# Kernel tuning notes

Measured on AMD Instinct MI355X. Metric: run time of the kernel, lower is better.

Reference implementation:

```python
import jax, jax.numpy as jnp
import numpy as np

B, T, NT, H, L, F, NH, R = 2, 1024, 30, 1024, 8, 2816, 16, 16
HD = H // NH
LORA_SCALE = 32.0 / 16.0  # lora_alpha / r
CLAMP = 10.0
EPS = 1e-6


def _rms(x, w):
    return x * jax.lax.rsqrt(jnp.mean(x * x, axis=-1, keepdims=True) + EPS) * w


def _rope(x):
    # x: [B,T,NH,HD] -- LLaMA rotary embedding
    half = HD // 2
    inv_freq = 1.0 / (10000.0 ** (jnp.arange(0, half, dtype=jnp.float32) / half))
    ang = jnp.arange(x.shape[1], dtype=jnp.float32)[:, None] * inv_freq  # [T,half]
    cos = jnp.concatenate([jnp.cos(ang), jnp.cos(ang)], -1)[None, :, None, :]
    sin = jnp.concatenate([jnp.sin(ang), jnp.sin(ang)], -1)[None, :, None, :]
    x1, x2 = x[..., :half], x[..., half:]
    return x * cos + jnp.concatenate([-x2, x1], -1) * sin


def _lora(x, W, A, Bm):
    # W: [in,out], A: [r,in], Bm: [out,r]  (dequantized base + LoRA update)
    return x @ W + ((x @ A.T) @ Bm.T) * LORA_SCALE


def setup_inputs():
    key = jax.random.key(0)
    ks = jax.random.split(key, 16)
    n = lambda k, s, sc=0.02: jax.random.normal(k, s, jnp.float32) * sc
    return {
        'x': jax.random.normal(ks[0], (B, T, NT), jnp.float32),
        'temperature': jnp.float32(1.0),
        'state_W': n(ks[1], (NT, H), 0.1),
        'state_b': jnp.zeros((H,), jnp.float32),
        'ln1': jnp.ones((L, H), jnp.float32),
        'ln2': jnp.ones((L, H), jnp.float32),
        'Wqkv': n(ks[2], (L, 3, H, H)),
        'Aqkv': n(ks[3], (L, 3, R, H)),
        'Bqkv': n(ks[4], (L, 3, H, R)),
        'Wo': n(ks[5], (L, H, H)),
        'Ao': n(ks[6], (L, R, H)),
        'Bo': n(ks[7], (L, H, R)),
        'Wgu': n(ks[8], (L, 2, H, F)),
        'Agu': n(ks[9], (L, 2, R, H)),
        'Bgu': n(ks[10], (L, 2, F, R)),
        'Wd': n(ks[11], (L, F, H)),
        'Ad': n(ks[12], (L, R, F)),
        'Bd': n(ks[13], (L, H, R)),
        'ln_f': jnp.ones((H,), jnp.float32),
        'head_W': n(ks[14], (H, NT + 1), 0.01),
        'head_b': jnp.zeros((NT + 1,), jnp.float32),
    }


def reference(x, temperature, state_W, state_b, ln1, ln2, Wqkv, Aqkv, Bqkv,
              Wo, Ao, Bo, Wgu, Agu, Bgu, Wd, Ad, Bd, ln_f, head_W, head_b):
    causal = jnp.tril(jnp.ones((T, T), bool))

    def layer(h, p):
        l1, l2, wqkv, aqkv, bqkv, wo, ao, bo, wgu, agu, bgu, wd, ad, bd = p
        hn = _rms(h, l1)
        qkv = jnp.einsum('bth,khd->kbtd', hn, wqkv)
        qkv = qkv + jnp.einsum('kbtr,kdr->kbtd',
                               jnp.einsum('bth,krh->kbtr', hn, aqkv), bqkv) * LORA_SCALE
        q = _rope(qkv[0].reshape(B, T, NH, HD))
        k = _rope(qkv[1].reshape(B, T, NH, HD))
        v = qkv[2].reshape(B, T, NH, HD)
        scores = jnp.einsum('bqhd,bkhd->bhqk', q, k) / np.sqrt(HD).astype(np.float32)
        scores = jnp.where(causal, scores, jnp.float32(-1e9))
        probs = jax.nn.softmax(scores, axis=-1)
        att = jnp.einsum('bhqk,bkhd->bqhd', probs, v).reshape(B, T, H)
        h = h + _lora(att, wo, ao, bo)
        hn2 = _rms(h, l2)
        gu = jnp.einsum('bth,khf->kbtf', hn2, wgu)
        gu = gu + jnp.einsum('kbtr,kfr->kbtf',
                             jnp.einsum('bth,krh->kbtr', hn2, agu), bgu) * LORA_SCALE
        act = jax.nn.silu(gu[0]) * gu[1]
        h = h + _lora(act, wd, ad, bd)
        return h, None

    h = x @ state_W + state_b  # state encoder -> inputs_embeds
    h, _ = jax.lax.scan(layer, h, (ln1, ln2, Wqkv, Aqkv, Bqkv, Wo, Ao, Bo,
                                   Wgu, Agu, Bgu, Wd, Ad, Bd))
    latent = _rms(h, ln_f)  # last hidden state
    logits = latent @ head_W + head_b
    logits_clamped = jnp.clip(logits, -CLAMP, CLAMP)
    portfolio_weights = jax.nn.softmax(logits_clamped / temperature, axis=-1)
    return portfolio_weights, logits_clamped
```

## Files before the change

kernel.cpp:

```cpp
#include <hip/hip_runtime.h>
#include <hip/hip_bf16.h>
#include <cstdint>

#define B_    2
#define T_    1024
#define NT_   30
#define H_    1024
#define L_    8
#define F_    2816
#define NH_   16
#define R_    16
#define HD_   64
#define M_    2048
#define NTP1_ 31

typedef unsigned short u16;
typedef short  s16x8 __attribute__((ext_vector_type(8)));
typedef unsigned short u16x4 __attribute__((ext_vector_type(4)));
typedef unsigned short u16x8 __attribute__((ext_vector_type(8)));
typedef float  f32x4 __attribute__((ext_vector_type(4)));

__device__ __forceinline__ u16 f2bf(float f){
  __hip_bfloat16 h = __float2bfloat16(f);
  return __builtin_bit_cast(unsigned short, h);
}
__device__ __forceinline__ float bf2f(u16 u){
  uint32_t v = (uint32_t)u << 16;
  return __builtin_bit_cast(float, v);
}

__device__ __forceinline__ void async16(const void* g, void* l){
  __builtin_amdgcn_global_load_lds((const __attribute__((address_space(1))) void*)g,
                                   (__attribute__((address_space(3))) void*)l, 16, 0, 0);
}

__global__ __launch_bounds__(256, 3) void fold_kernel(
    const float* __restrict__ W, const float* __restrict__ A,
    const float* __restrict__ Bm, u16* __restrict__ Wt,
    int K, int N, long strW, long strA, long strB, long strWt)
{
  const int mat = blockIdx.z;
  W  += (long)mat * strW;  A  += (long)mat * strA;
  Bm += (long)mat * strB;  Wt += (long)mat * strWt;
  const int k0 = blockIdx.x * 64, n0 = blockIdx.y * 64;
  __shared__ float Wt_s[64][65];
  __shared__ float As[16][64];
  __shared__ float Bs[64][20];
  const int tid = threadIdx.x;
  {
    const int kr = tid >> 4;
    const int n4 = (tid & 15) * 4;
    #pragma unroll
    for (int p = 0; p < 4; p++){
      int krow = p * 16 + kr;
      float4 w = *(const float4*)(W + (long)(k0 + krow) * N + n0 + n4);
      Wt_s[n4+0][krow] = w.x; Wt_s[n4+1][krow] = w.y;
      Wt_s[n4+2][krow] = w.z; Wt_s[n4+3][krow] = w.w;
    }
    const int r = tid >> 4, kc = (tid & 15) * 4;
    *(float4*)&As[r][kc] = *(const float4*)(A + (long)r * K + k0 + kc);
    const int nb = tid >> 2, r4 = (tid & 3) * 4;
    float4 b = *(const float4*)(Bm + (long)(n0 + nb) * 16 + r4);
    Bs[nb][r4+0]=b.x; Bs[nb][r4+1]=b.y; Bs[nb][r4+2]=b.z; Bs[nb][r4+3]=b.w;
  }
  __syncthreads();
  const int ko = (tid & 7) * 8;
  const int na = tid >> 3;
  float bq0[16], bq1[16];
  #pragma unroll
  for (int c = 0; c < 4; c++){
    *(float4*)&bq0[c*4] = *(const float4*)&Bs[na][c*4];
    *(float4*)&bq1[c*4] = *(const float4*)&Bs[na+32][c*4];
  }
  float l0[8] = {}, l1[8] = {};
  #pragma unroll
  for (int r = 0; r < 16; r++){
    float a[8];
    *(float4*)&a[0] = *(const float4*)&As[r][ko];
    *(float4*)&a[4] = *(const float4*)&As[r][ko+4];
    #pragma unroll
    for (int j = 0; j < 8; j++){
      l0[j] += a[j] * bq0[r];
      l1[j] += a[j] * bq1[r];
    }
  }
  u16x8 o0, o1;
  #pragma unroll
  for (int j = 0; j < 8; j++){
    o0[j] = f2bf(Wt_s[na][ko+j]    + 2.0f * l0[j]);
    o1[j] = f2bf(Wt_s[na+32][ko+j] + 2.0f * l1[j]);
  }
  *(u16x8*)(Wt + (long)(n0+na)*K    + k0 + ko) = o0;
  *(u16x8*)(Wt + (long)(n0+na+32)*K + k0 + ko) = o1;
}

__global__ __launch_bounds__(256) void embed_kernel(
    const float* __restrict__ x, const float* __restrict__ sw,
    const float* __restrict__ sb, float* __restrict__ h)
{
  const int m = blockIdx.x;
  const float* xr = x + (long)m * NT_;
  for (int jj = threadIdx.x; jj < H_; jj += 256){
    float acc = sb[jj];
    #pragma unroll
    for (int i = 0; i < NT_; i++) acc += xr[i] * sw[i * H_ + jj];
    h[(long)m * H_ + jj] = acc;
  }
}

__global__ __launch_bounds__(256) void rms_kernel(
    float* __restrict__ hsrc, const u16* __restrict__ pb,
    const float* __restrict__ w, u16* __restrict__ outp, int nparts)
{
  const int m = blockIdx.x, t = threadIdx.x;
  float4 v = ((const float4*)(hsrc + (long)m * H_))[t];
  if (nparts){
    for (int k = 0; k < nparts; k++){
      u16x4 a = *(const u16x4*)(pb + (long)k * M_ * H_ + (long)m * H_ + t * 4);
      v.x += bf2f(a[0]); v.y += bf2f(a[1]); v.z += bf2f(a[2]); v.w += bf2f(a[3]);
    }
    ((float4*)(hsrc + (long)m * H_))[t] = v;
  }
  float ss = v.x*v.x + v.y*v.y + v.z*v.z + v.w*v.w;
  #pragma unroll
  for (int off = 32; off >= 1; off >>= 1) ss += __shfl_xor(ss, off);
  __shared__ float red[4];
  if ((t & 63) == 0) red[t >> 6] = ss;
  __syncthreads();
  const float scale = rsqrtf((red[0]+red[1]+red[2]+red[3]) * (1.0f/H_) + 1e-6f);
  const float4 wv = ((const float4*)w)[t];
  u16x4 o;
  o[0] = f2bf(v.x*scale*wv.x); o[1] = f2bf(v.y*scale*wv.y);
  o[2] = f2bf(v.z*scale*wv.z); o[3] = f2bf(v.w*scale*wv.w);
  *(u16x4*)(outp + (long)m * H_ + t * 4) = o;
}

template<int OUTBF>
__global__ __launch_bounds__(256, 3) void gemm_bt(
    const u16* __restrict__ Ag, const u16* __restrict__ Btg, void* __restrict__ Cptr,
    int Ndim, int Kstride, int Ksteps, long zsC)
{
  const int z = blockIdx.z, Z = (int)gridDim.z;
  const int kb = Ksteps / Z, rem = Ksteps % Z;
  const int sblk = (z < rem) ? z * (kb + 1) : rem * (kb + 1) + (z - rem) * kb;
  const int klen = (kb + (z < rem ? 1 : 0)) * 64;
  Ag  += (long)sblk * 64;
  Btg += (long)sblk * 64;
  const int m0 = blockIdx.x * 128, n0 = blockIdx.y * 128;
  __shared__ alignas(16) u16 As[128 * 64];
  __shared__ alignas(16) u16 Bs[128 * 64];
  const int tid = threadIdx.x;
  const int wave = tid >> 6, lane = tid & 63;
  const int wm = (wave & 1) * 64, wn = (wave >> 1) * 64;
  const int fr = lane & 15, quad = lane >> 4;

  f32x4 acc[4][4] = {};

  for (int kt = 0; kt < klen; kt += 64){
    __syncthreads();
    #pragma unroll
    for (int c = 0; c < 4; c++){
      int lin = c * 256 + tid;
      int row = lin >> 3, p = lin & 7;
      int gc = ((p ^ (row & 7)) * 8);
      async16(Ag  + (long)(m0 + row) * Kstride + kt + gc, As + lin * 8);
      async16(Btg + (long)(n0 + row) * Kstride + kt + gc, Bs + lin * 8);
    }
    __syncthreads();
    #pragma unroll
    for (int kk = 0; kk < 2; kk++){
      s16x8 af[4], bg[4];
      #pragma unroll
      for (int i = 0; i < 4; i++){
        int rA = wm + i * 16 + fr;
        af[i] = *(const s16x8*)(As + rA * 64 + (((kk*4 + quad) ^ (rA & 7)) * 8));
        int rB = wn + i * 16 + fr;
        bg[i] = *(const s16x8*)(Bs + rB * 64 + (((kk*4 + quad) ^ (rB & 7)) * 8));
      }
      #pragma unroll
      for (int i = 0; i < 4; i++)
        #pragma unroll
        for (int j = 0; j < 4; j++)
          acc[i][j] = __builtin_amdgcn_mfma_f32_16x16x32_bf16(af[i], bg[j], acc[i][j], 0, 0, 0);
    }
  }
  #pragma unroll
  for (int i = 0; i < 4; i++){
    int row0 = m0 + wm + i * 16 + quad * 4;
    #pragma unroll
    for (int j = 0; j < 4; j++){
      int col = n0 + wn + j * 16 + fr;
      #pragma unroll
      for (int r = 0; r < 4; r++){
        long idx = (long)(row0 + r) * Ndim + col;
        if (OUTBF){
          u16* C = (u16*)Cptr + (long)blockIdx.z * zsC;
          C[idx] = f2bf(acc[i][j][r]);
        } else {
          float* C = (float*)Cptr + (long)blockIdx.z * zsC;
          C[idx] = acc[i][j][r];
        }
      }
    }
  }
}

__global__ __launch_bounds__(256, 3) void gemm_qkv(
    const u16* __restrict__ Ag, const u16* __restrict__ Btg,
    u16* __restrict__ qr, u16* __restrict__ kr, u16* __restrict__ vt)
{
  const int m0 = blockIdx.x * 128, n0 = blockIdx.y * 128;
  __shared__ alignas(16) u16 As[128 * 64];
  __shared__ alignas(16) u16 Bs[128 * 64];
  const int tid = threadIdx.x;
  const int wave = tid >> 6, lane = tid & 63;
  const int wm = (wave & 1) * 64, wn = (wave >> 1) * 64;
  const int fr = lane & 15, quad = lane >> 4;

  f32x4 acc[4][4] = {};

  for (int kt = 0; kt < H_; kt += 64){
    __syncthreads();
    #pragma unroll
    for (int c = 0; c < 4; c++){
      int lin = c * 256 + tid;
      int row = lin >> 3, p = lin & 7;
      int gc = ((p ^ (row & 7)) * 8);
      async16(Ag  + (long)(m0 + row) * H_ + kt + gc, As + lin * 8);
      async16(Btg + (long)(n0 + row) * H_ + kt + gc, Bs + lin * 8);
    }
    __syncthreads();
    #pragma unroll
    for (int kk = 0; kk < 2; kk++){
      s16x8 af[4], bg[4];
      #pragma unroll
      for (int i = 0; i < 4; i++){
        int rA = wm + i * 16 + fr;
        af[i] = *(const s16x8*)(As + rA * 64 + (((kk*4 + quad) ^ (rA & 7)) * 8));
        int rB = wn + i * 16 + fr;
        bg[i] = *(const s16x8*)(Bs + rB * 64 + (((kk*4 + quad) ^ (rB & 7)) * 8));
      }
      #pragma unroll
      for (int i = 0; i < 4; i++)
        #pragma unroll
        for (int j = 0; j < 4; j++)
          acc[i][j] = __builtin_amdgcn_mfma_f32_16x16x32_bf16(af[i], bg[j], acc[i][j], 0, 0, 0);
    }
  }
  const int sel  = n0 >> 10;
  const int nloc = (n0 & 1023) + wn;
  const int hh   = nloc >> 6;
  if (sel == 2){
    #pragma unroll
    for (int i = 0; i < 4; i++){
      int row0 = m0 + wm + i * 16 + quad * 4;
      int b = row0 >> 10, t0 = row0 & 1023;
      #pragma unroll
      for (int j = 0; j < 4; j++){
        int d = j * 16 + fr;
        u16x4 o;
        #pragma unroll
        for (int r = 0; r < 4; r++) o[r] = f2bf(acc[i][j][r]);
        *(u16x4*)(vt + ((long)((b * NH_ + hh) * HD_ + d)) * T_ + t0) = o;
      }
    }
  } else {
    u16* dst = sel ? kr : qr;
    #pragma unroll
    for (int i = 0; i < 4; i++){
      int row0 = m0 + wm + i * 16 + quad * 4;
      int b = row0 >> 10;
      #pragma unroll
      for (int j = 0; j < 2; j++){
        int d1 = j * 16 + fr;
        float freq = exp2f((float)d1 * (-13.287712379549449f / 32.0f));
        #pragma unroll
        for (int r = 0; r < 4; r++){
          int t = (row0 + r) & 1023;
          float x1 = acc[i][j][r], x2 = acc[i][j + 2][r];
          float sn, cs; __sincosf((float)t * freq, &sn, &cs);
          long base = ((long)(b * NH_ + hh) * T_ + t) * HD_;
          dst[base + d1]      = f2bf(x1 * cs - x2 * sn);
          dst[base + d1 + 32] = f2bf(x2 * cs + x1 * sn);
        }
      }
    }
  }
}

__global__ __launch_bounds__(256, 3) void gemm_gu(
    const u16* __restrict__ Ag, const u16* __restrict__ Bgw,
    const u16* __restrict__ Buw, u16* __restrict__ actb)
{
  const int m0 = blockIdx.x * 128, n0 = blockIdx.y * 64;
  __shared__ alignas(16) u16 As[128 * 64];
  __shared__ alignas(16) u16 Bg_[64 * 64];
  __shared__ alignas(16) u16 Bu_[64 * 64];
  const int tid = threadIdx.x;
  const int wave = tid >> 6, lane = tid & 63;
  const int wm = (wave & 1) * 64, wn = (wave >> 1) * 32;
  const int fr = lane & 15, quad = lane >> 4;

  f32x4 accg[4][2] = {}, accu[4][2] = {};

  for (int kt = 0; kt < H_; kt += 64){
    __syncthreads();
    #pragma unroll
    for (int c = 0; c < 4; c++){
      int lin = c * 256 + tid;
      int row = lin >> 3, p = lin & 7;
      async16(Ag + (long)(m0 + row) * H_ + kt + ((p ^ (row & 7)) * 8), As + lin * 8);
    }
    #pragma unroll
    for (int c = 0; c < 2; c++){
      int lin = c * 256 + tid;
      int row = lin >> 3, p = lin & 7;
      int gc = ((p ^ (row & 7)) * 8);
      async16(Bgw + (long)(n0 + row) * H_ + kt + gc, Bg_ + lin * 8);
      async16(Buw + (long)(n0 + row) * H_ + kt + gc, Bu_ + lin * 8);
    }
    __syncthreads();
    #pragma unroll
    for (int kk = 0; kk < 2; kk++){
      s16x8 af[4], bg[2], bu[2];
      #pragma unroll
      for (int i = 0; i < 4; i++){
        int rA = wm + i * 16 + fr;
        af[i] = *(const s16x8*)(As + rA * 64 + (((kk*4 + quad) ^ (rA & 7)) * 8));
      }
      #pragma unroll
      for (int j = 0; j < 2; j++){
        int rB = wn + j * 16 + fr;
        bg[j] = *(const s16x8*)(Bg_ + rB * 64 + (((kk*4 + quad) ^ (rB & 7)) * 8));
        bu[j] = *(const s16x8*)(Bu_ + rB * 64 + (((kk*4 + quad) ^ (rB & 7)) * 8));
      }
      #pragma unroll
      for (int i = 0; i < 4; i++)
        #pragma unroll
        for (int j = 0; j < 2; j++){
          accg[i][j] = __builtin_amdgcn_mfma_f32_16x16x32_bf16(af[i], bg[j], accg[i][j], 0, 0, 0);
          accu[i][j] = __builtin_amdgcn_mfma_f32_16x16x32_bf16(af[i], bu[j], accu[i][j], 0, 0, 0);
        }
    }
  }
  #pragma unroll
  for (int i = 0; i < 4; i++){
    int row0 = m0 + wm + i * 16 + quad * 4;
    #pragma unroll
    for (int j = 0; j < 2; j++){
      int col = n0 + wn + j * 16 + fr;
      #pragma unroll
      for (int r = 0; r < 4; r++){
        float g = accg[i][j][r], u = accu[i][j][r];
        float act = g / (1.0f + __expf(-g)) * u;
        actb[(long)(row0 + r) * F_ + col] = f2bf(act);
      }
    }
  }
}

__global__ __launch_bounds__(256, 2) void attn_kernel(
    const u16* __restrict__ qr, const u16* __restrict__ kr,
    const u16* __restrict__ vt, u16* __restrict__ att)
{
  const int bh = blockIdx.y;
  const int b = bh >> 4, hh = bh & 15;
  const int qt = blockIdx.x;
  __shared__ alignas(16) u16 Qs[64 * 64];
  __shared__ alignas(16) u16 Ks[128 * 64];
  __shared__ alignas(16) u16 Vs[64 * 128];
  __shared__ alignas(16) u16 Ps[64 * 136];
  const int tid = threadIdx.x;
  const int wave = tid >> 6, lane = tid & 63, fr = lane & 15, quad = lane >> 4;
  const int wrow = wave * 16;
  const u16* kgb = kr + (long)bh * T_ * HD_;
  const u16* vgb = vt + (long)bh * HD_ * T_;

  const u16* qg = qr + ((long)bh * T_ + qt * 64) * HD_;
  #pragma unroll
  for (int c = 0; c < 2; c++){
    int lin = c * 256 + tid, row = lin >> 3, p = lin & 7;
    async16(qg + row * HD_ + ((p ^ (row & 7)) * 8), Qs + lin * 8);
  }
  f32x4 o_acc[4] = {};
  float m_r[4] = {-1e30f, -1e30f, -1e30f, -1e30f};
  float l_r[4] = {};
  const int kmax = (qt * 64 + 63) >> 7;

  for (int kt = 0; kt <= kmax; kt++){
    __syncthreads();
    const u16* kg = kgb + (long)kt * 128 * HD_;
    #pragma unroll
    for (int c = 0; c < 4; c++){
      int lin = c * 256 + tid, row = lin >> 3, p = lin & 7;
      async16(kg + row * HD_ + ((p ^ (row & 7)) * 8), Ks + lin * 8);
    }
    #pragma unroll
    for (int c = 0; c < 4; c++){
      int lin = c * 256 + tid, row = lin >> 4, p = lin & 15;
      async16(vgb + (long)row * T_ + kt * 128 + ((p ^ (row & 15)) * 8), Vs + lin * 8);
    }
    __syncthreads();

    f32x4 s[8] = {};
    s16x8 aq[2];
    {
      int rA = wrow + fr;
      #pragma unroll
      for (int kk = 0; kk < 2; kk++)
        aq[kk] = *(const s16x8*)(Qs + rA * 64 + (((kk*4 + quad) ^ (rA & 7)) * 8));
    }
    #pragma unroll
    for (int ik = 0; ik < 8; ik++){
      #pragma unroll
      for (int kk = 0; kk < 2; kk++){
        int rB = ik * 16 + fr;
        s16x8 bk = *(const s16x8*)(Ks + rB * 64 + (((kk*4 + quad) ^ (rB & 7)) * 8));
        s[ik] = __builtin_amdgcn_mfma_f32_16x16x32_bf16(aq[kk], bk, s[ik], 0, 0, 0);
      }
    }
    const bool diag = (kt == kmax);
    #pragma unroll
    for (int r = 0; r < 4; r++){
      const int qgi = qt * 64 + wrow + quad * 4 + r;
      float tmax = -1e30f;
      #pragma unroll
      for (int ik = 0; ik < 8; ik++){
        float v = s[ik][r] * 0.125f;
        if (diag && (kt * 128 + ik * 16 + fr) > qgi) v = -1e9f;
        s[ik][r] = v;
        tmax = fmaxf(tmax, v);
      }
      #pragma unroll
      for (int off = 8; off >= 1; off >>= 1) tmax = fmaxf(tmax, __shfl_xor(tmax, off));
      const float mnew = fmaxf(m_r[r], tmax);
      const float alpha = __expf(m_r[r] - mnew);
      m_r[r] = mnew;
      float ts = 0.0f;
      const int prow = wrow + quad * 4 + r;
      #pragma unroll
      for (int ik = 0; ik < 8; ik++){
        float p = __expf(s[ik][r] - mnew);
        ts += p;
        Ps[prow * 136 + ik * 16 + fr] = f2bf(p);
      }
      #pragma unroll
      for (int off = 8; off >= 1; off >>= 1) ts += __shfl_xor(ts, off);
      l_r[r] = l_r[r] * alpha + ts;
      #pragma unroll
      for (int jd = 0; jd < 4; jd++) o_acc[jd][r] *= alpha;
    }
    #pragma unroll
    for (int kk2 = 0; kk2 < 4; kk2++){
      s16x8 ap = *(const s16x8*)(Ps + (wrow + fr) * 136 + kk2 * 32 + quad * 8);
      #pragma unroll
      for (int jd = 0; jd < 4; jd++){
        int rV = jd * 16 + fr;
        s16x8 bv = *(const s16x8*)(Vs + rV * 128 + (((kk2*4 + quad) ^ (rV & 15)) * 8));
        o_acc[jd] = __builtin_amdgcn_mfma_f32_16x16x32_bf16(ap, bv, o_acc[jd], 0, 0, 0);
      }
    }
  }
  #pragma unroll
  for (int r = 0; r < 4; r++){
    const int t_loc = qt * 64 + wrow + quad * 4 + r;
    const long rowbase = ((long)b * T_ + t_loc) * H_ + hh * HD_;
    const float inv = 1.0f / l_r[r];
    #pragma unroll
    for (int jd = 0; jd < 4; jd++)
      att[rowbase + jd * 16 + fr] = f2bf(o_acc[jd][r] * inv);
  }
}

__global__ __launch_bounds__(256) void head_kernel(
    const float* __restrict__ hsrc, const u16* __restrict__ pb,
    const float* __restrict__ lnf, const float* __restrict__ hw, const float* __restrict__ hb,
    const float* __restrict__ temp, float* __restrict__ outp)
{
  const int m = blockIdx.x, t = threadIdx.x;
  __shared__ float lat[H_];
  __shared__ float red[4];
  __shared__ float part[8][32];
  float4 v = ((const float4*)(hsrc + (long)m * H_))[t];
  #pragma unroll
  for (int k = 0; k < 4; k++){
    u16x4 a = *(const u16x4*)(pb + (long)k * M_ * H_ + (long)m * H_ + t * 4);
    v.x += bf2f(a[0]); v.y += bf2f(a[1]); v.z += bf2f(a[2]); v.w += bf2f(a[3]);
  }
  float ss = v.x*v.x + v.y*v.y + v.z*v.z + v.w*v.w;
  #pragma unroll
  for (int off = 32; off >= 1; off >>= 1) ss += __shfl_xor(ss, off);
  if ((t & 63) == 0) red[t >> 6] = ss;
  __syncthreads();
  const float scale = rsqrtf((red[0]+red[1]+red[2]+red[3]) * (1.0f/H_) + 1e-6f);
  const float4 wv = ((const float4*)lnf)[t];
  lat[t*4+0] = v.x*scale*wv.x;  lat[t*4+1] = v.y*scale*wv.y;
  lat[t*4+2] = v.z*scale*wv.z;  lat[t*4+3] = v.w*scale*wv.w;
  __syncthreads();
  const int j = t & 31, seg = t >> 5;
  float pp = 0.0f;
  if (j < 31){
    const float* wp = hw + j;
    for (int k = seg * 128; k < seg * 128 + 128; k++) pp += lat[k] * wp[(long)k * 31];
  }
  part[seg][j] = pp;
  __syncthreads();
  if (t < 32){
    float dot = 0.0f;
    #pragma unroll
    for (int s2 = 0; s2 < 8; s2++) dot += part[s2][t];
    const float logit = (t < 31) ? dot + hb[t] : -1e30f;
    const float lc = fminf(fmaxf(logit, -10.0f), 10.0f);
    const float z = (t < 31) ? lc / temp[0] : -1e30f;
    float mx = z;
    #pragma unroll
    for (int off = 16; off >= 1; off >>= 1) mx = fmaxf(mx, __shfl_xor(mx, off, 32));
    const float e = (t < 31) ? __expf(z - mx) : 0.0f;
    float sum = e;
    #pragma unroll
    for (int off = 16; off >= 1; off >>= 1) sum += __shfl_xor(sum, off, 32);
    if (t < 31){
      outp[(long)m * NTP1_ + t] = e / sum;
      outp[(long)M_ * NTP1_ + (long)m * NTP1_ + t] = lc;
    }
  }
}

extern "C" void kernel_launch(void* const* d_in, const int* in_sizes, int n_in,
                              void* d_out, int out_size, void* d_ws, size_t ws_size,
                              hipStream_t stream) {
  const float* x    = (const float*)d_in[0];
  const float* temp = (const float*)d_in[1];
  const float* sW   = (const float*)d_in[2];
  const float* sb   = (const float*)d_in[3];
  const float* ln1  = (const float*)d_in[4];
  const float* ln2  = (const float*)d_in[5];
  const float* Wqkv = (const float*)d_in[6];
  const float* Aqkv = (const float*)d_in[7];
  const float* Bqkv = (const float*)d_in[8];
  const float* Wo   = (const float*)d_in[9];
  const float* Ao   = (const float*)d_in[10];
  const float* Bo   = (const float*)d_in[11];
  const float* Wgu  = (const float*)d_in[12];
  const float* Agu  = (const float*)d_in[13];
  const float* Bgu  = (const float*)d_in[14];
  const float* Wd   = (const float*)d_in[15];
  const float* Ad   = (const float*)d_in[16];
  const float* Bd   = (const float*)d_in[17];
  const float* lnf  = (const float*)d_in[18];
  const float* hW   = (const float*)d_in[19];
  const float* hb   = (const float*)d_in[20];
  float* out = (float*)d_out;

  uint8_t* ws = (uint8_t*)d_ws;
  size_t off = 0;
  auto alloc = [&](size_t bytes) -> void* {
    void* p = ws + off;
    off += (bytes + 255) & ~(size_t)255;
    return p;
  };
  u16*   wt_qkv = (u16*)  alloc((size_t)L_ * 3 * H_ * H_ * 2);
  u16*   wt_o   = (u16*)  alloc((size_t)L_ * H_ * H_ * 2);
  u16*   wt_gu  = (u16*)  alloc((size_t)L_ * 2 * F_ * H_ * 2);
  u16*   wt_d   = (u16*)  alloc((size_t)L_ * H_ * F_ * 2);
  float* h      = (float*)alloc((size_t)M_ * H_ * 4);
  u16*   hn     = (u16*)  alloc((size_t)M_ * H_ * 2);
  u16*   pb16   = (u16*)  alloc((size_t)4 * M_ * H_ * 2);
  u16*   qr     = (u16*)  alloc((size_t)M_ * H_ * 2);
  u16*   krr    = (u16*)  alloc((size_t)M_ * H_ * 2);
  u16*   vtb    = (u16*)  alloc((size_t)M_ * H_ * 2);
  u16*   attb   = (u16*)  alloc((size_t)M_ * H_ * 2);
  u16*   actb   = (u16*)  alloc((size_t)M_ * F_ * 2);

  fold_kernel<<<dim3(16, 16, L_ * 3), 256, 0, stream>>>(Wqkv, Aqkv, Bqkv, wt_qkv,
      H_, H_, (long)H_ * H_, (long)R_ * H_, (long)H_ * R_, (long)H_ * H_);
  fold_kernel<<<dim3(16, 16, L_), 256, 0, stream>>>(Wo, Ao, Bo, wt_o,
      H_, H_, (long)H_ * H_, (long)R_ * H_, (long)H_ * R_, (long)H_ * H_);
  fold_kernel<<<dim3(16, 44, L_ * 2), 256, 0, stream>>>(Wgu, Agu, Bgu, wt_gu,
      H_, F_, (long)H_ * F_, (long)R_ * H_, (long)F_ * R_, (long)F_ * H_);
  fold_kernel<<<dim3(44, 16, L_), 256, 0, stream>>>(Wd, Ad, Bd, wt_d,
      F_, H_, (long)F_ * H_, (long)R_ * F_, (long)H_ * R_, (long)H_ * F_);

  embed_kernel<<<M_, 256, 0, stream>>>(x, sW, sb, h);

  for (int l = 0; l < L_; l++){
    rms_kernel<<<M_, 256, 0, stream>>>(h, pb16, ln1 + (long)l * H_, hn, l > 0 ? 4 : 0);
    gemm_qkv<<<dim3(16, 24), 256, 0, stream>>>(hn, wt_qkv + (long)l * 3 * H_ * H_,
        qr, krr, vtb);
    attn_kernel<<<dim3(16, B_ * NH_), 256, 0, stream>>>(qr, krr, vtb, attb);
    gemm_bt<1><<<dim3(16, 8, 2), 256, 0, stream>>>(attb, wt_o + (long)l * H_ * H_,
        pb16, H_, H_, 16, (long)M_ * H_);
    rms_kernel<<<M_, 256, 0, stream>>>(h, pb16, ln2 + (long)l * H_, hn, 2);
    gemm_gu<<<dim3(16, 44), 256, 0, stream>>>(hn,
        wt_gu + (long)l * 2 * F_ * H_, wt_gu + (long)l * 2 * F_ * H_ + (long)F_ * H_, actb);
    gemm_bt<1><<<dim3(16, 8, 4), 256, 0, stream>>>(actb, wt_d + (long)l * H_ * F_,
        pb16, H_, F_, 44, (long)M_ * H_);
  }

  head_kernel<<<M_, 256, 0, stream>>>(h, pb16, lnf, hW, hb, temp, out);
}
```

Baseline: 1.554 ms.

## Fuse prep kernels, batch RMS rows, stream Q/V from global in attention

Merges the four LoRA weight-fold launches and the embedding into one prep kernel with a flat block index. RMS norm now handles four rows per block. Attention loads Q straight into registers and reads V fragments directly from global instead of staging them in LDS, which cuts LDS use so occupancy can go to 3. It also reverses the q-tile order for the second batch to balance the causal workload and raises wave priority around the MFMA sections. Out-projection split-K rises from 2 to 4, and the following RMS sums 4 partials to match. Uncoalesced global V reads may cost more than the LDS staging they replace.

```diff
diff --git a/kernel.cpp b/kernel.cpp
--- a/kernel.cpp
+++ b/kernel.cpp
@@ -34,18 +34,17 @@
                                    (__attribute__((address_space(3))) void*)l, 16, 0, 0);
 }
 
-__global__ __launch_bounds__(256, 3) void fold_kernel(
+struct FoldSmem {
+  float Wt_s[64][65];
+  float As[16][64];
+  float Bs[64][20];
+};
+
+__device__ __forceinline__ void fold_tile(
     const float* __restrict__ W, const float* __restrict__ A,
     const float* __restrict__ Bm, u16* __restrict__ Wt,
-    int K, int N, long strW, long strA, long strB, long strWt)
-{
-  const int mat = blockIdx.z;
-  W  += (long)mat * strW;  A  += (long)mat * strA;
-  Bm += (long)mat * strB;  Wt += (long)mat * strWt;
-  const int k0 = blockIdx.x * 64, n0 = blockIdx.y * 64;
-  __shared__ float Wt_s[64][65];
-  __shared__ float As[16][64];
-  __shared__ float Bs[64][20];
+    int K, int N, int k0, int n0, FoldSmem& sm)
+{
   const int tid = threadIdx.x;
   {
     const int kr = tid >> 4;
@@ -54,14 +53,14 @@
     for (int p = 0; p < 4; p++){
       int krow = p * 16 + kr;
       float4 w = *(const float4*)(W + (long)(k0 + krow) * N + n0 + n4);
-      Wt_s[n4+0][krow] = w.x; Wt_s[n4+1][krow] = w.y;
-      Wt_s[n4+2][krow] = w.z; Wt_s[n4+3][krow] = w.w;
+      sm.Wt_s[n4+0][krow] = w.x; sm.Wt_s[n4+1][krow] = w.y;
+      sm.Wt_s[n4+2][krow] = w.z; sm.Wt_s[n4+3][krow] = w.w;
     }
     const int r = tid >> 4, kc = (tid & 15) * 4;
-    *(float4*)&As[r][kc] = *(const float4*)(A + (long)r * K + k0 + kc);
+    *(float4*)&sm.As[r][kc] = *(const float4*)(A + (long)r * K + k0 + kc);
     const int nb = tid >> 2, r4 = (tid & 3) * 4;
     float4 b = *(const float4*)(Bm + (long)(n0 + nb) * 16 + r4);
-    Bs[nb][r4+0]=b.x; Bs[nb][r4+1]=b.y; Bs[nb][r4+2]=b.z; Bs[nb][r4+3]=b.w;
+    sm.Bs[nb][r4+0]=b.x; sm.Bs[nb][r4+1]=b.y; sm.Bs[nb][r4+2]=b.z; sm.Bs[nb][r4+3]=b.w;
   }
   __syncthreads();
   const int ko = (tid & 7) * 8;
@@ -69,15 +68,15 @@
   float bq0[16], bq1[16];
   #pragma unroll
   for (int c = 0; c < 4; c++){
-    *(float4*)&bq0[c*4] = *(const float4*)&Bs[na][c*4];
-    *(float4*)&bq1[c*4] = *(const float4*)&Bs[na+32][c*4];
+    *(float4*)&bq0[c*4] = *(const float4*)&sm.Bs[na][c*4];
+    *(float4*)&bq1[c*4] = *(const float4*)&sm.Bs[na+32][c*4];
   }
   float l0[8] = {}, l1[8] = {};
   #pragma unroll
   for (int r = 0; r < 16; r++){
     float a[8];
-    *(float4*)&a[0] = *(const float4*)&As[r][ko];
-    *(float4*)&a[4] = *(const float4*)&As[r][ko+4];
+    *(float4*)&a[0] = *(const float4*)&sm.As[r][ko];
+    *(float4*)&a[4] = *(const float4*)&sm.As[r][ko+4];
     #pragma unroll
     for (int j = 0; j < 8; j++){
       l0[j] += a[j] * bq0[r];
@@ -87,24 +86,60 @@
   u16x8 o0, o1;
   #pragma unroll
   for (int j = 0; j < 8; j++){
-    o0[j] = f2bf(Wt_s[na][ko+j]    + 2.0f * l0[j]);
-    o1[j] = f2bf(Wt_s[na+32][ko+j] + 2.0f * l1[j]);
+    o0[j] = f2bf(sm.Wt_s[na][ko+j]    + 2.0f * l0[j]);
+    o1[j] = f2bf(sm.Wt_s[na+32][ko+j] + 2.0f * l1[j]);
   }
   *(u16x8*)(Wt + (long)(n0+na)*K    + k0 + ko) = o0;
   *(u16x8*)(Wt + (long)(n0+na+32)*K + k0 + ko) = o1;
 }
 
-__global__ __launch_bounds__(256) void embed_kernel(
+__global__ __launch_bounds__(256, 4) void prep_kernel(
+    const float* __restrict__ Wqkv, const float* __restrict__ Aqkv,
+    const float* __restrict__ Bqkv, u16* __restrict__ wt_qkv,
+    const float* __restrict__ Wo, const float* __restrict__ Ao,
+    const float* __restrict__ Bo, u16* __restrict__ wt_o,
+    const float* __restrict__ Wgu, const float* __restrict__ Agu,
+    const float* __restrict__ Bgu, u16* __restrict__ wt_gu,
+    const float* __restrict__ Wd, const float* __restrict__ Ad,
+    const float* __restrict__ Bd, u16* __restrict__ wt_d,
     const float* __restrict__ x, const float* __restrict__ sw,
     const float* __restrict__ sb, float* __restrict__ h)
 {
-  const int m = blockIdx.x;
-  const float* xr = x + (long)m * NT_;
-  for (int jj = threadIdx.x; jj < H_; jj += 256){
-    float acc = sb[jj];
-    #pragma unroll
-    for (int i = 0; i < NT_; i++) acc += xr[i] * sw[i * H_ + jj];
-    h[(long)m * H_ + jj] = acc;
+  __shared__ FoldSmem sm;
+  const int id = blockIdx.x;
+  if (id < 25088){
+    const float *W, *A, *Bm; u16* Wt; int K, N, k0, n0;
+    if (id < 6144){
+      int z = id >> 8, r = id & 255;
+      W = Wqkv + (long)z * 1048576; A = Aqkv + (long)z * 16384;
+      Bm = Bqkv + (long)z * 16384; Wt = wt_qkv + (long)z * 1048576;
+      K = 1024; N = 1024; k0 = (r & 15) * 64; n0 = (r >> 4) * 64;
+    } else if (id < 8192){
+      int t = id - 6144; int z = t >> 8, r = t & 255;
+      W = Wo + (long)z * 1048576; A = Ao + (long)z * 16384;
+      Bm = Bo + (long)z * 16384;  Wt = wt_o + (long)z * 1048576;
+      K = 1024; N = 1024; k0 = (r & 15) * 64; n0 = (r >> 4) * 64;
+    } else if (id < 19456){
+      int t = id - 8192; int z = t / 704, r = t % 704;
+      W = Wgu + (long)z * 2883584; A = Agu + (long)z * 16384;
+      Bm = Bgu + (long)z * 45056;  Wt = wt_gu + (long)z * 2883584;
+      K = 1024; N = 2816; k0 = (r % 16) * 64; n0 = (r / 16) * 64;
+    } else {
+      int t = id - 19456; int z = t / 704, r = t % 704;
+      W = Wd + (long)z * 2883584; A = Ad + (long)z * 45056;
+      Bm = Bd + (long)z * 16384;  Wt = wt_d + (long)z * 2883584;
+      K = 2816; N = 1024; k0 = (r % 44) * 64; n0 = (r / 44) * 64;
+    }
+    fold_tile(W, A, Bm, Wt, K, N, k0, n0, sm);
+  } else {
+    const int m = id - 25088;
+    const float* xr = x + (long)m * NT_;
+    for (int jj = threadIdx.x; jj < H_; jj += 256){
+      float acc = sb[jj];
+      #pragma unroll
+      for (int i = 0; i < NT_; i++) acc += xr[i] * sw[i * H_ + jj];
+      h[(long)m * H_ + jj] = acc;
+    }
   }
 }
 
@@ -112,27 +147,31 @@
     float* __restrict__ hsrc, const u16* __restrict__ pb,
     const float* __restrict__ w, u16* __restrict__ outp, int nparts)
 {
-  const int m = blockIdx.x, t = threadIdx.x;
-  float4 v = ((const float4*)(hsrc + (long)m * H_))[t];
-  if (nparts){
-    for (int k = 0; k < nparts; k++){
-      u16x4 a = *(const u16x4*)(pb + (long)k * M_ * H_ + (long)m * H_ + t * 4);
-      v.x += bf2f(a[0]); v.y += bf2f(a[1]); v.z += bf2f(a[2]); v.w += bf2f(a[3]);
-    }
-    ((float4*)(hsrc + (long)m * H_))[t] = v;
-  }
-  float ss = v.x*v.x + v.y*v.y + v.z*v.z + v.w*v.w;
-  #pragma unroll
-  for (int off = 32; off >= 1; off >>= 1) ss += __shfl_xor(ss, off);
+  const int t = threadIdx.x;
   __shared__ float red[4];
-  if ((t & 63) == 0) red[t >> 6] = ss;
-  __syncthreads();
-  const float scale = rsqrtf((red[0]+red[1]+red[2]+red[3]) * (1.0f/H_) + 1e-6f);
   const float4 wv = ((const float4*)w)[t];
-  u16x4 o;
-  o[0] = f2bf(v.x*scale*wv.x); o[1] = f2bf(v.y*scale*wv.y);
-  o[2] = f2bf(v.z*scale*wv.z); o[3] = f2bf(v.w*scale*wv.w);
-  *(u16x4*)(outp + (long)m * H_ + t * 4) = o;
+  for (int it = 0; it < 4; it++){
+    const int m = blockIdx.x * 4 + it;
+    float4 v = ((const float4*)(hsrc + (long)m * H_))[t];
+    if (nparts){
+      for (int k = 0; k < nparts; k++){
+        u16x4 a = *(const u16x4*)(pb + (long)k * M_ * H_ + (long)m * H_ + t * 4);
+        v.x += bf2f(a[0]); v.y += bf2f(a[1]); v.z += bf2f(a[2]); v.w += bf2f(a[3]);
+      }
+      ((float4*)(hsrc + (long)m * H_))[t] = v;
+    }
+    float ss = v.x*v.x + v.y*v.y + v.z*v.z + v.w*v.w;
+    #pragma unroll
+    for (int off = 32; off >= 1; off >>= 1) ss += __shfl_xor(ss, off);
+    if ((t & 63) == 0) red[t >> 6] = ss;
+    __syncthreads();
+    const float scale = rsqrtf((red[0]+red[1]+red[2]+red[3]) * (1.0f/H_) + 1e-6f);
+    u16x4 o;
+    o[0] = f2bf(v.x*scale*wv.x); o[1] = f2bf(v.y*scale*wv.y);
+    o[2] = f2bf(v.z*scale*wv.z); o[3] = f2bf(v.w*scale*wv.w);
+    *(u16x4*)(outp + (long)m * H_ + t * 4) = o;
+    __syncthreads();
+  }
 }
 
 template<int OUTBF>
@@ -359,29 +398,27 @@
   }
 }
 
-__global__ __launch_bounds__(256, 2) void attn_kernel(
+__global__ __launch_bounds__(256, 3) void attn_kernel(
     const u16* __restrict__ qr, const u16* __restrict__ kr,
     const u16* __restrict__ vt, u16* __restrict__ att)
 {
   const int bh = blockIdx.y;
   const int b = bh >> 4, hh = bh & 15;
-  const int qt = blockIdx.x;
-  __shared__ alignas(16) u16 Qs[64 * 64];
+  const int qt = b ? (15 - (int)blockIdx.x) : (int)blockIdx.x;
   __shared__ alignas(16) u16 Ks[128 * 64];
-  __shared__ alignas(16) u16 Vs[64 * 128];
   __shared__ alignas(16) u16 Ps[64 * 136];
   const int tid = threadIdx.x;
   const int wave = tid >> 6, lane = tid & 63, fr = lane & 15, quad = lane >> 4;
   const int wrow = wave * 16;
   const u16* kgb = kr + (long)bh * T_ * HD_;
   const u16* vgb = vt + (long)bh * HD_ * T_;
-
-  const u16* qg = qr + ((long)bh * T_ + qt * 64) * HD_;
-  #pragma unroll
-  for (int c = 0; c < 2; c++){
-    int lin = c * 256 + tid, row = lin >> 3, p = lin & 7;
-    async16(qg + row * HD_ + ((p ^ (row & 7)) * 8), Qs + lin * 8);
-  }
+  const u16* qg  = qr + ((long)bh * T_ + qt * 64) * HD_;
+
+  s16x8 aq[2];
+  #pragma unroll
+  for (int kk = 0; kk < 2; kk++)
+    aq[kk] = *(const s16x8*)(qg + (wrow + fr) * HD_ + kk * 32 + quad * 8);
+
   f32x4 o_acc[4] = {};
   float m_r[4] = {-1e30f, -1e30f, -1e30f, -1e30f};
   float l_r[4] = {};
@@ -395,21 +432,10 @@
       int lin = c * 256 + tid, row = lin >> 3, p = lin & 7;
       async16(kg + row * HD_ + ((p ^ (row & 7)) * 8), Ks + lin * 8);
     }
-    #pragma unroll
-    for (int c = 0; c < 4; c++){
-      int lin = c * 256 + tid, row = lin >> 4, p = lin & 15;
-      async16(vgb + (long)row * T_ + kt * 128 + ((p ^ (row & 15)) * 8), Vs + lin * 8);
-    }
     __syncthreads();
 
     f32x4 s[8] = {};
-    s16x8 aq[2];
-    {
-      int rA = wrow + fr;
-      #pragma unroll
-      for (int kk = 0; kk < 2; kk++)
-        aq[kk] = *(const s16x8*)(Qs + rA * 64 + (((kk*4 + quad) ^ (rA & 7)) * 8));
-    }
+    __builtin_amdgcn_s_setprio(1);
     #pragma unroll
     for (int ik = 0; ik < 8; ik++){
       #pragma unroll
@@ -419,6 +445,7 @@
         s[ik] = __builtin_amdgcn_mfma_f32_16x16x32_bf16(aq[kk], bk, s[ik], 0, 0, 0);
       }
     }
+    __builtin_amdgcn_s_setprio(0);
     const bool diag = (kt == kmax);
     #pragma unroll
     for (int r = 0; r < 4; r++){
@@ -450,16 +477,17 @@
       #pragma unroll
       for (int jd = 0; jd < 4; jd++) o_acc[jd][r] *= alpha;
     }
+    __builtin_amdgcn_s_setprio(1);
     #pragma unroll
     for (int kk2 = 0; kk2 < 4; kk2++){
       s16x8 ap = *(const s16x8*)(Ps + (wrow + fr) * 136 + kk2 * 32 + quad * 8);
       #pragma unroll
       for (int jd = 0; jd < 4; jd++){
-        int rV = jd * 16 + fr;
-        s16x8 bv = *(const s16x8*)(Vs + rV * 128 + (((kk2*4 + quad) ^ (rV & 15)) * 8));
+        s16x8 bv = *(const s16x8*)(vgb + (long)(jd * 16 + fr) * T_ + kt * 128 + kk2 * 32 + quad * 8);
         o_acc[jd] = __builtin_amdgcn_mfma_f32_16x16x32_bf16(ap, bv, o_acc[jd], 0, 0, 0);
       }
     }
+    __builtin_amdgcn_s_setprio(0);
   }
   #pragma unroll
   for (int r = 0; r < 4; r++){
@@ -572,25 +600,18 @@
   u16*   attb   = (u16*)  alloc((size_t)M_ * H_ * 2);
   u16*   actb   = (u16*)  alloc((size_t)M_ * F_ * 2);
 
-  fold_kernel<<<dim3(16, 16, L_ * 3), 256, 0, stream>>>(Wqkv, Aqkv, Bqkv, wt_qkv,
-      H_, H_, (long)H_ * H_, (long)R_ * H_, (long)H_ * R_, (long)H_ * H_);
-  fold_kernel<<<dim3(16, 16, L_), 256, 0, stream>>>(Wo, Ao, Bo, wt_o,
-      H_, H_, (long)H_ * H_, (long)R_ * H_, (long)H_ * R_, (long)H_ * H_);
-  fold_kernel<<<dim3(16, 44, L_ * 2), 256, 0, stream>>>(Wgu, Agu, Bgu, wt_gu,
-      H_, F_, (long)H_ * F_, (long)R_ * H_, (long)F_ * R_, (long)F_ * H_);
-  fold_kernel<<<dim3(44, 16, L_), 256, 0, stream>>>(Wd, Ad, Bd, wt_d,
-      F_, H_, (long)F_ * H_, (long)R_ * F_, (long)H_ * R_, (long)H_ * F_);
-
-  embed_kernel<<<M_, 256, 0, stream>>>(x, sW, sb, h);
+  prep_kernel<<<27136, 256, 0, stream>>>(
+      Wqkv, Aqkv, Bqkv, wt_qkv, Wo, Ao, Bo, wt_o,
+      Wgu, Agu, Bgu, wt_gu, Wd, Ad, Bd, wt_d, x, sW, sb, h);
 
   for (int l = 0; l < L_; l++){
-    rms_kernel<<<M_, 256, 0, stream>>>(h, pb16, ln1 + (long)l * H_, hn, l > 0 ? 4 : 0);
+    rms_kernel<<<M_ / 4, 256, 0, stream>>>(h, pb16, ln1 + (long)l * H_, hn, l > 0 ? 4 : 0);
     gemm_qkv<<<dim3(16, 24), 256, 0, stream>>>(hn, wt_qkv + (long)l * 3 * H_ * H_,
         qr, krr, vtb);
     attn_kernel<<<dim3(16, B_ * NH_), 256, 0, stream>>>(qr, krr, vtb, attb);
-    gemm_bt<1><<<dim3(16, 8, 2), 256, 0, stream>>>(attb, wt_o + (long)l * H_ * H_,
+    gemm_bt<1><<<dim3(16, 8, 4), 256, 0, stream>>>(attb, wt_o + (long)l * H_ * H_,
         pb16, H_, H_, 16, (long)M_ * H_);
-    rms_kernel<<<M_, 256, 0, stream>>>(h, pb16, ln2 + (long)l * H_, hn, 2);
+    rms_kernel<<<M_ / 4, 256, 0, stream>>>(h, pb16, ln2 + (long)l * H_, hn, 4);
     gemm_gu<<<dim3(16, 44), 256, 0, stream>>>(hn,
         wt_gu + (long)l * 2 * F_ * H_, wt_gu + (long)l * 2 * F_ * H_ + (long)F_ * H_, actb);
     gemm_bt<1><<<dim3(16, 8, 4), 256, 0, stream>>>(actb, wt_d + (long)l * H_ * F_,
```

Result: slower. 1.625 ms (+4.6%).
